# Performance work log

Measured on AMD Instinct MI355X. Metric: run time of the kernel, lower is better.

## Reference

```python
import jax, jax.numpy as jnp
import numpy as np

N_DRUG = 10000
N_DIS = 10000
IN_UNITS = 256
N_EDGES = 1000000


def setup_inputs() -> dict:
    key = jax.random.key(0)
    ks = jax.random.split(key, 10)
    # Kaiming-uniform-ish init like torch Linear defaults
    def lin_w(k, fan_in, fan_out):
        bound = 1.0 / np.sqrt(fan_in)
        return jax.random.uniform(k, (fan_in, fan_out), jnp.float32, -bound, bound)
    return {
        "drug_feat": jax.random.normal(ks[0], (N_DRUG, IN_UNITS), jnp.float32),
        "dis_feat": jax.random.normal(ks[1], (N_DIS, IN_UNITS), jnp.float32),
        "src_idx": jax.random.randint(ks[2], (N_EDGES,), 0, N_DRUG, jnp.int64),
        "dst_idx": jax.random.randint(ks[3], (N_EDGES,), 0, N_DIS, jnp.int64),
        "W1": lin_w(ks[4], 2 * IN_UNITS, 128),
        "b1": jnp.zeros((128,), jnp.float32),
        "W2": lin_w(ks[5], 128, 64),
        "b2": jnp.zeros((64,), jnp.float32),
        "W3": lin_w(ks[6], 64, 1),
        "b3": jnp.zeros((1,), jnp.float32),
    }


def reference(drug_feat, dis_feat, src_idx, dst_idx, W1, b1, W2, b2, W3, b3):
    # apply_edges: gather src (drug) and dst (disease) features, concat -> [E, 2*in_units]
    m = jnp.concatenate([drug_feat[src_idx], dis_feat[dst_idx]], axis=1)
    # 3-layer MLP (dropout = identity in eval)
    h = jax.nn.relu(m @ W1 + b1)
    h = jax.nn.relu(h @ W2 + b2)
    out = h @ W3 + b3  # [E, 1]
    return out
```

## Files before the change

### kernel.cpp

```cpp
#include <hip/hip_runtime.h>
#include <hip/hip_fp16.h>

#define IN_UNITS 256
#define H1 128
#define H2 64

typedef _Float16 f16x8 __attribute__((ext_vector_type(8)));
typedef float f32x4 __attribute__((ext_vector_type(4)));

union HV { uint4 u; f16x8 v; unsigned short s[8]; };

static __device__ __forceinline__ unsigned short h2bits(_Float16 x) {
    union { _Float16 h; unsigned short u; } c; c.h = x; return c.u;
}

__global__ __launch_bounds__(256)
void proj_kernel(
    const float* __restrict__ drug_feat, const float* __restrict__ dis_feat,
    const float* __restrict__ W1, const float* __restrict__ b1,
    unsigned short* __restrict__ drug_h, unsigned short* __restrict__ dis_h,
    int n_rows)
{
    int t = threadIdx.x, lane = t & 63, wave = t >> 6;
    int side = wave >> 1, ch = wave & 1;
    int mtile = blockIdx.x;
    const float* feat = side ? dis_feat : drug_feat;
    unsigned short* outb = side ? dis_h : drug_h;

    int row = mtile * 16 + (lane & 15);
    if (row >= n_rows) row = n_rows - 1;
    int kb = (lane >> 4) * 8;

    float4 fx[16];
    #pragma unroll
    for (int i = 0; i < 16; ++i)
        fx[i] = *(const float4*)(feat + (size_t)row * IN_UNITS + (i >> 1) * 32 + kb + (i & 1) * 4);

    const float* w1base = W1 + (size_t)(side * IN_UNITS + (lane >> 4) * 8) * H1
                             + ch * 64 + (lane & 15);

    f32x4 acc[4];
    #pragma unroll
    for (int nt = 0; nt < 4; ++nt) acc[nt] = (f32x4){0.f, 0.f, 0.f, 0.f};

    #pragma unroll
    for (int ks = 0; ks < 8; ++ks) {
        float4 x0 = fx[ks * 2], x1 = fx[ks * 2 + 1];
        f16x8 a;
        a[0] = (_Float16)x0.x; a[1] = (_Float16)x0.y;
        a[2] = (_Float16)x0.z; a[3] = (_Float16)x0.w;
        a[4] = (_Float16)x1.x; a[5] = (_Float16)x1.y;
        a[6] = (_Float16)x1.z; a[7] = (_Float16)x1.w;
        #pragma unroll
        for (int nt = 0; nt < 4; ++nt) {
            HV bb;
            #pragma unroll
            for (int j = 0; j < 8; ++j)
                bb.s[j] = h2bits((_Float16)w1base[(size_t)(ks * 32 + j) * H1 + nt * 16]);
            acc[nt] = __builtin_amdgcn_mfma_f32_16x16x32_f16(a, bb.v, acc[nt], 0, 0, 0);
        }
    }

    #pragma unroll
    for (int nt = 0; nt < 4; ++nt) {
        int col = ch * 64 + nt * 16 + (lane & 15);
        float bb = side ? b1[col] : 0.f;
        #pragma unroll
        for (int r = 0; r < 4; ++r) {
            int rr = mtile * 16 + (lane >> 4) * 4 + r;
            if (rr < n_rows)
                outb[(size_t)rr * H1 + col] = h2bits((_Float16)(acc[nt][r] + bb));
        }
    }
}

__global__ __launch_bounds__(256) __attribute__((amdgpu_waves_per_eu(6, 8)))
void edge_kernel(
    const unsigned short* __restrict__ drug_h, const unsigned short* __restrict__ dis_h,
    const int* __restrict__ src_idx, const int* __restrict__ dst_idx,
    const float* __restrict__ W2, const float* __restrict__ b2,
    const float* __restrict__ W3, const float* __restrict__ b3,
    float* __restrict__ out, int n_edges)
{
    __shared__ uint4 w2s[1024];

    int t = threadIdx.x, lane = t & 63;
    int wave = t >> 6;
    int e0 = (blockIdx.x * 4 + wave) * 32;
    int emax = n_edges - 1;

    int i0 = e0 + (lane & 15);      if (i0 > emax) i0 = emax;
    int i1 = e0 + 16 + (lane & 15); if (i1 > emax) i1 = emax;
    int s0 = src_idx[i0], d0 = dst_idx[i0];
    int s1 = src_idx[i1], d1 = dst_idx[i1];

    #pragma unroll
    for (int i = 0; i < 4; ++i) {
        int slot = i * 256 + t;
        int f = slot >> 6, l = slot & 63;
        int ks = f >> 2, nt = f & 3;
        int row0 = ks * 32 + (l >> 4) * 8;
        int col  = nt * 16 + (l & 15);
        HV v;
        #pragma unroll
        for (int j = 0; j < 8; ++j)
            v.s[j] = h2bits((_Float16)W2[(size_t)(row0 + j) * H2 + col]);
        w2s[slot] = v.u;
    }

    int kb = (lane >> 4) * 8;
    const uint4* pa0 = (const uint4*)(drug_h + s0 * H1 + kb);
    const uint4* pc0 = (const uint4*)(dis_h  + d0 * H1 + kb);
    const uint4* pa1 = (const uint4*)(drug_h + s1 * H1 + kb);
    const uint4* pc1 = (const uint4*)(dis_h  + d1 * H1 + kb);
    uint4 ga0[4], gc0[4], ga1[4], gc1[4];
    #pragma unroll
    for (int ks = 0; ks < 4; ++ks) {
        ga0[ks] = pa0[ks * 4];
        gc0[ks] = pc0[ks * 4];
        ga1[ks] = pa1[ks * 4];
        gc1[ks] = pc1[ks * 4];
    }

    float b2v[4], w3v[4];
    #pragma unroll
    for (int nt = 0; nt < 4; ++nt) {
        int col = (lane & 15) + nt * 16;
        b2v[nt] = b2[col];
        w3v[nt] = W3[col];
    }
    float b3v = b3[0];

    __syncthreads();

    f32x4 acc[2][4];
    #pragma unroll
    for (int mt = 0; mt < 2; ++mt)
        #pragma unroll
        for (int nt = 0; nt < 4; ++nt)
            acc[mt][nt] = (f32x4){0.f, 0.f, 0.f, 0.f};

    #pragma unroll
    for (int ks = 0; ks < 4; ++ks) {
        HV a0, c0, a1, c1;
        a0.u = ga0[ks]; c0.u = gc0[ks];
        a1.u = ga1[ks]; c1.u = gc1[ks];
        f16x8 zero = (f16x8)(_Float16)0;
        f16x8 r0v = __builtin_elementwise_max(a0.v + c0.v, zero);
        f16x8 r1v = __builtin_elementwise_max(a1.v + c1.v, zero);
        #pragma unroll
        for (int nt = 0; nt < 4; ++nt) {
            HV bb; bb.u = w2s[(ks * 4 + nt) * 64 + lane];
            acc[0][nt] = __builtin_amdgcn_mfma_f32_16x16x32_f16(r0v, bb.v, acc[0][nt], 0, 0, 0);
            acc[1][nt] = __builtin_amdgcn_mfma_f32_16x16x32_f16(r1v, bb.v, acc[1][nt], 0, 0, 0);
        }
    }

    #pragma unroll
    for (int mt = 0; mt < 2; ++mt) {
        float part[4];
        #pragma unroll
        for (int r = 0; r < 4; ++r) {
            float p = 0.f;
            #pragma unroll
            for (int nt = 0; nt < 4; ++nt)
                p += fmaxf(acc[mt][nt][r] + b2v[nt], 0.f) * w3v[nt];
            part[r] = p;
        }
        #pragma unroll
        for (int off = 1; off <= 8; off <<= 1)
            #pragma unroll
            for (int r = 0; r < 4; ++r)
                part[r] += __shfl_xor(part[r], off, 64);
        if ((lane & 15) == 0) {
            #pragma unroll
            for (int r = 0; r < 4; ++r) {
                int e = e0 + mt * 16 + (lane >> 4) * 4 + r;
                if (e < n_edges) out[e] = part[r] + b3v;
            }
        }
    }
}

extern "C" void kernel_launch(void* const* d_in, const int* in_sizes, int n_in,
                              void* d_out, int out_size, void* d_ws, size_t ws_size,
                              hipStream_t stream) {
    const float* drug_feat = (const float*)d_in[0];
    const float* dis_feat  = (const float*)d_in[1];
    const int*   src_idx   = (const int*)d_in[2];
    const int*   dst_idx   = (const int*)d_in[3];
    const float* W1 = (const float*)d_in[4];
    const float* b1 = (const float*)d_in[5];
    const float* W2 = (const float*)d_in[6];
    const float* b2 = (const float*)d_in[7];
    const float* W3 = (const float*)d_in[8];
    const float* b3 = (const float*)d_in[9];
    float* out = (float*)d_out;

    int n_edges = in_sizes[2];
    int n_drug = in_sizes[0] / IN_UNITS;

    unsigned short* drug_h = (unsigned short*)d_ws;
    unsigned short* dis_h  = drug_h + (size_t)n_drug * H1;

    int mtiles = (n_drug + 15) / 16;
    proj_kernel<<<mtiles, 256, 0, stream>>>(
        drug_feat, dis_feat, W1, b1, drug_h, dis_h, n_drug);

    int edge_blocks = (n_edges + 127) / 128;
    edge_kernel<<<edge_blocks, 256, 0, stream>>>(
        drug_h, dis_h, src_idx, dst_idx, W2, b2, W3, b3, out, n_edges);
}
```

Measured before the change: 198.1 us.

## Split projection K across waves and use 512-thread edge blocks with one tile per wave

The projection kernel now launches separate blocks for the drug and disease sides and splits the K dimension across wave pairs. Partial sums are combined through shared memory, which halves per-thread register use and doubles the block count. The edge kernel now gives each wave 16 edges instead of 32 and uses 512-thread blocks, so the shared W2 conversion is amortised over more waves. Row gathers are issued before the W2 staging so they overlap it. The cost is an extra LDS round-trip and barrier in the projection, and less per-wave instruction-level parallelism in the edge MFMA loop.

```diff
diff --git a/kernel.cpp b/kernel.cpp
--- a/kernel.cpp
+++ b/kernel.cpp
@@ -19,11 +19,15 @@
     const float* __restrict__ drug_feat, const float* __restrict__ dis_feat,
     const float* __restrict__ W1, const float* __restrict__ b1,
     unsigned short* __restrict__ drug_h, unsigned short* __restrict__ dis_h,
-    int n_rows)
+    int mtiles, int n_rows)
 {
+    __shared__ f32x4 lacc[8][64];
+
     int t = threadIdx.x, lane = t & 63, wave = t >> 6;
-    int side = wave >> 1, ch = wave & 1;
-    int mtile = blockIdx.x;
+    int ch = wave & 1, kh = wave >> 1;
+    int b = blockIdx.x;
+    int side = b >= mtiles;
+    int mtile = b - side * mtiles;
     const float* feat = side ? dis_feat : drug_feat;
     unsigned short* outb = side ? dis_h : drug_h;
 
@@ -31,12 +35,13 @@
     if (row >= n_rows) row = n_rows - 1;
     int kb = (lane >> 4) * 8;
 
-    float4 fx[16];
-    #pragma unroll
-    for (int i = 0; i < 16; ++i)
-        fx[i] = *(const float4*)(feat + (size_t)row * IN_UNITS + (i >> 1) * 32 + kb + (i & 1) * 4);
-
-    const float* w1base = W1 + (size_t)(side * IN_UNITS + (lane >> 4) * 8) * H1
+    const float* fp = feat + (size_t)row * IN_UNITS + kh * 128 + kb;
+    float4 fx[8];
+    #pragma unroll
+    for (int i = 0; i < 8; ++i)
+        fx[i] = *(const float4*)(fp + (i >> 1) * 32 + (i & 1) * 4);
+
+    const float* w1base = W1 + (size_t)(side * IN_UNITS + kh * 128 + kb) * H1
                              + ch * 64 + (lane & 15);
 
     f32x4 acc[4];
@@ -44,7 +49,7 @@
     for (int nt = 0; nt < 4; ++nt) acc[nt] = (f32x4){0.f, 0.f, 0.f, 0.f};
 
     #pragma unroll
-    for (int ks = 0; ks < 8; ++ks) {
+    for (int ks = 0; ks < 4; ++ks) {
         float4 x0 = fx[ks * 2], x1 = fx[ks * 2 + 1];
         f16x8 a;
         a[0] = (_Float16)x0.x; a[1] = (_Float16)x0.y;
@@ -61,20 +66,29 @@
         }
     }
 
-    #pragma unroll
-    for (int nt = 0; nt < 4; ++nt) {
-        int col = ch * 64 + nt * 16 + (lane & 15);
-        float bb = side ? b1[col] : 0.f;
-        #pragma unroll
-        for (int r = 0; r < 4; ++r) {
-            int rr = mtile * 16 + (lane >> 4) * 4 + r;
-            if (rr < n_rows)
-                outb[(size_t)rr * H1 + col] = h2bits((_Float16)(acc[nt][r] + bb));
-        }
-    }
-}
-
-__global__ __launch_bounds__(256) __attribute__((amdgpu_waves_per_eu(6, 8)))
+    if (kh == 1) {
+        #pragma unroll
+        for (int nt = 0; nt < 4; ++nt) lacc[ch * 4 + nt][lane] = acc[nt];
+    }
+    __syncthreads();
+    if (kh == 0) {
+        #pragma unroll
+        for (int nt = 0; nt < 4; ++nt) {
+            f32x4 p = lacc[ch * 4 + nt][lane];
+            int col = ch * 64 + nt * 16 + (lane & 15);
+            float bbias = side ? b1[col] : 0.f;
+            #pragma unroll
+            for (int r = 0; r < 4; ++r) {
+                int rr = mtile * 16 + (lane >> 4) * 4 + r;
+                if (rr < n_rows)
+                    outb[(size_t)rr * H1 + col] =
+                        h2bits((_Float16)(acc[nt][r] + p[r] + bbias));
+            }
+        }
+    }
+}
+
+__global__ __launch_bounds__(512) __attribute__((amdgpu_waves_per_eu(6, 8)))
 void edge_kernel(
     const unsigned short* __restrict__ drug_h, const unsigned short* __restrict__ dis_h,
     const int* __restrict__ src_idx, const int* __restrict__ dst_idx,
@@ -84,19 +98,27 @@
 {
     __shared__ uint4 w2s[1024];
 
-    int t = threadIdx.x, lane = t & 63;
-    int wave = t >> 6;
-    int e0 = (blockIdx.x * 4 + wave) * 32;
+    int t = threadIdx.x, lane = t & 63, wave = t >> 6;
+    int e0 = blockIdx.x * 128 + wave * 16;
     int emax = n_edges - 1;
 
-    int i0 = e0 + (lane & 15);      if (i0 > emax) i0 = emax;
-    int i1 = e0 + 16 + (lane & 15); if (i1 > emax) i1 = emax;
+    int i0 = e0 + (lane & 15);
+    if (i0 > emax) i0 = emax;
     int s0 = src_idx[i0], d0 = dst_idx[i0];
-    int s1 = src_idx[i1], d1 = dst_idx[i1];
-
-    #pragma unroll
-    for (int i = 0; i < 4; ++i) {
-        int slot = i * 256 + t;
+
+    int kb = (lane >> 4) * 8;
+    const uint4* pa = (const uint4*)(drug_h + s0 * H1 + kb);
+    const uint4* pc = (const uint4*)(dis_h  + d0 * H1 + kb);
+    uint4 ga[4], gc[4];
+    #pragma unroll
+    for (int ks = 0; ks < 4; ++ks) {
+        ga[ks] = pa[ks * 4];
+        gc[ks] = pc[ks * 4];
+    }
+
+    #pragma unroll
+    for (int i = 0; i < 2; ++i) {
+        int slot = i * 512 + t;
         int f = slot >> 6, l = slot & 63;
         int ks = f >> 2, nt = f & 3;
         int row0 = ks * 32 + (l >> 4) * 8;
@@ -107,19 +129,23 @@
             v.s[j] = h2bits((_Float16)W2[(size_t)(row0 + j) * H2 + col]);
         w2s[slot] = v.u;
     }
-
-    int kb = (lane >> 4) * 8;
-    const uint4* pa0 = (const uint4*)(drug_h + s0 * H1 + kb);
-    const uint4* pc0 = (const uint4*)(dis_h  + d0 * H1 + kb);
-    const uint4* pa1 = (const uint4*)(drug_h + s1 * H1 + kb);
-    const uint4* pc1 = (const uint4*)(dis_h  + d1 * H1 + kb);
-    uint4 ga0[4], gc0[4], ga1[4], gc1[4];
+    __syncthreads();
+
+    f32x4 acc[4];
+    #pragma unroll
+    for (int nt = 0; nt < 4; ++nt) acc[nt] = (f32x4){0.f, 0.f, 0.f, 0.f};
+
     #pragma unroll
     for (int ks = 0; ks < 4; ++ks) {
-        ga0[ks] = pa0[ks * 4];
-        gc0[ks] = pc0[ks * 4];
-        ga1[ks] = pa1[ks * 4];
-        gc1[ks] = pc1[ks * 4];
+        HV a, c;
+        a.u = ga[ks]; c.u = gc[ks];
+        f16x8 zero = (f16x8)(_Float16)0;
+        f16x8 rv = __builtin_elementwise_max(a.v + c.v, zero);
+        #pragma unroll
+        for (int nt = 0; nt < 4; ++nt) {
+            HV bb; bb.u = w2s[(ks * 4 + nt) * 64 + lane];
+            acc[nt] = __builtin_amdgcn_mfma_f32_16x16x32_f16(rv, bb.v, acc[nt], 0, 0, 0);
+        }
     }
 
     float b2v[4], w3v[4];
@@ -131,53 +157,25 @@
     }
     float b3v = b3[0];
 
-    __syncthreads();
-
-    f32x4 acc[2][4];
-    #pragma unroll
-    for (int mt = 0; mt < 2; ++mt)
+    float part[4];
+    #pragma unroll
+    for (int r = 0; r < 4; ++r) {
+        float p = 0.f;
         #pragma unroll
         for (int nt = 0; nt < 4; ++nt)
-            acc[mt][nt] = (f32x4){0.f, 0.f, 0.f, 0.f};
-
-    #pragma unroll
-    for (int ks = 0; ks < 4; ++ks) {
-        HV a0, c0, a1, c1;
-        a0.u = ga0[ks]; c0.u = gc0[ks];
-        a1.u = ga1[ks]; c1.u = gc1[ks];
-        f16x8 zero = (f16x8)(_Float16)0;
-        f16x8 r0v = __builtin_elementwise_max(a0.v + c0.v, zero);
-        f16x8 r1v = __builtin_elementwise_max(a1.v + c1.v, zero);
-        #pragma unroll
-        for (int nt = 0; nt < 4; ++nt) {
-            HV bb; bb.u = w2s[(ks * 4 + nt) * 64 + lane];
-            acc[0][nt] = __builtin_amdgcn_mfma_f32_16x16x32_f16(r0v, bb.v, acc[0][nt], 0, 0, 0);
-            acc[1][nt] = __builtin_amdgcn_mfma_f32_16x16x32_f16(r1v, bb.v, acc[1][nt], 0, 0, 0);
-        }
-    }
-
-    #pragma unroll
-    for (int mt = 0; mt < 2; ++mt) {
-        float part[4];
+            p += fmaxf(acc[nt][r] + b2v[nt], 0.f) * w3v[nt];
+        part[r] = p;
+    }
+    #pragma unroll
+    for (int off = 1; off <= 8; off <<= 1)
+        #pragma unroll
+        for (int r = 0; r < 4; ++r)
+            part[r] += __shfl_xor(part[r], off, 64);
+    if ((lane & 15) == 0) {
         #pragma unroll
         for (int r = 0; r < 4; ++r) {
-            float p = 0.f;
-            #pragma unroll
-            for (int nt = 0; nt < 4; ++nt)
-                p += fmaxf(acc[mt][nt][r] + b2v[nt], 0.f) * w3v[nt];
-            part[r] = p;
-        }
-        #pragma unroll
-        for (int off = 1; off <= 8; off <<= 1)
-            #pragma unroll
-            for (int r = 0; r < 4; ++r)
-                part[r] += __shfl_xor(part[r], off, 64);
-        if ((lane & 15) == 0) {
-            #pragma unroll
-            for (int r = 0; r < 4; ++r) {
-                int e = e0 + mt * 16 + (lane >> 4) * 4 + r;
-                if (e < n_edges) out[e] = part[r] + b3v;
-            }
+            int e = e0 + (lane >> 4) * 4 + r;
+            if (e < n_edges) out[e] = part[r] + b3v;
         }
     }
 }
@@ -204,10 +202,10 @@
     unsigned short* dis_h  = drug_h + (size_t)n_drug * H1;
 
     int mtiles = (n_drug + 15) / 16;
-    proj_kernel<<<mtiles, 256, 0, stream>>>(
-        drug_feat, dis_feat, W1, b1, drug_h, dis_h, n_drug);
+    proj_kernel<<<2 * mtiles, 256, 0, stream>>>(
+        drug_feat, dis_feat, W1, b1, drug_h, dis_h, mtiles, n_drug);
 
     int edge_blocks = (n_edges + 127) / 128;
-    edge_kernel<<<edge_blocks, 256, 0, stream>>>(
+    edge_kernel<<<edge_blocks, 512, 0, stream>>>(
         drug_h, dis_h, src_idx, dst_idx, W2, b2, W3, b3, out, n_edges);
 }
```

Result: faster. 168.1 us (-15.2%).
